# Performance work log

Measured on AMD Instinct MI355X. Metric: run time of the kernel, lower is better.

The kernel has to match this reference:

```python
import jax, jax.numpy as jnp
import numpy as np

N_NODES = 100000
N_EDGES = 1600000
D_IN, D_HID, N_CLS = 256, 128, 47


def setup_inputs() -> dict:
    key = jax.random.key(0)
    k = jax.random.split(key, 5)
    x = jax.random.normal(k[0], (N_NODES, D_IN), dtype=jnp.float32)
    edge_index = jax.random.randint(k[1], (2, N_EDGES), 0, N_NODES, dtype=jnp.int64)
    W1 = jax.random.normal(k[2], (D_IN, D_HID), dtype=jnp.float32) * 0.05
    b1 = jnp.zeros((D_HID,), dtype=jnp.float32)
    W2 = jax.random.normal(k[3], (D_HID, N_CLS), dtype=jnp.float32) * 0.05
    b2 = jnp.zeros((N_CLS,), dtype=jnp.float32)
    return {"x": x, "edge_index": edge_index, "W1": W1, "b1": b1, "W2": W2, "b2": b2}


def _gcn_conv(x, W, b, src, dst, norm, n):
    # PyG GCNConv: linear transform, normalized scatter-add aggregation, bias after
    h = x @ W                                   # [N, D_out]
    msg = h[src] * norm[:, None]                # gather over edges [E', D_out]
    agg = jax.ops.segment_sum(msg, dst, num_segments=n)
    return agg + b


def reference(x, edge_index, W1, b1, W2, b2):
    n = x.shape[0]
    loop = jnp.arange(n, dtype=edge_index.dtype)
    src = jnp.concatenate([edge_index[0], loop])  # add self-loops
    dst = jnp.concatenate([edge_index[1], loop])
    # symmetric normalization D^-1/2 (A+I) D^-1/2 (degree = in-degree incl. self-loop)
    deg = jax.ops.segment_sum(jnp.ones_like(dst, dtype=x.dtype), dst, num_segments=n)
    dinv = jnp.where(deg > 0, jax.lax.rsqrt(deg), 0.0)
    norm = dinv[src] * dinv[dst]                 # [E']
    h1 = jax.nn.relu(_gcn_conv(x, W1, b1, src, dst, norm, n))
    # dropout with training=False is identity
    out = _gcn_conv(h1, W2, b2, src, dst, norm, n)
    return out
```

## Files before the change

### kernel.cpp

```cpp
#include <hip/hip_runtime.h>
#include <hip/hip_bf16.h>

#define DIN 256
#define DHID 128
#define NCLS 47
#define BSHIFT 9
#define BNODES 512
#define NPART 256
#define BCAPS 9216
#define CHUNKE 6400

typedef __attribute__((ext_vector_type(8))) short short8;
typedef __attribute__((ext_vector_type(4))) float f32x4;

__device__ __forceinline__ short f2bf(float f) {
    __bf16 b = (__bf16)f;
    return __builtin_bit_cast(short, b);
}
__device__ __forceinline__ float bfu(unsigned int u) {
    return __uint_as_float(u << 16);
}
__device__ __forceinline__ float bfh(unsigned int u) {
    return __uint_as_float(u & 0xffff0000u);
}
__device__ __forceinline__ unsigned int pack2(float lo, float hi) {
    return (unsigned int)(unsigned short)f2bf(lo)
         | ((unsigned int)(unsigned short)f2bf(hi) << 16);
}
__device__ __forceinline__ void fma8(float* a, uint4 v, float d) {
    a[0] += d * bfu(v.x); a[1] += d * bfh(v.x);
    a[2] += d * bfu(v.y); a[3] += d * bfh(v.y);
    a[4] += d * bfu(v.z); a[5] += d * bfh(v.z);
    a[6] += d * bfu(v.w); a[7] += d * bfh(v.w);
}

__global__ __launch_bounds__(256) void k_prep_hist(const float* __restrict__ W1,
                                                   const float* __restrict__ W2,
                                                   short* __restrict__ W1s,
                                                   short* __restrict__ W2s,
                                                   const int* __restrict__ dst,
                                                   int* __restrict__ ghist,
                                                   int E, int NB, int chunk) {
    __shared__ int lh[256];
    int blk = blockIdx.x, t = threadIdx.x;
    if (blk < 16) {
        int tid = blk * 256 + t;
        int frag = tid >> 6, lane = tid & 63;
        int kt = frag >> 3, nt = frag & 7;
        int quad = lane >> 4, col = lane & 15;
        #pragma unroll
        for (int j = 0; j < 8; ++j) {
            int k = kt * 32 + quad * 8 + j;
            W1s[(size_t)tid * 8 + j] = f2bf(W1[k * DHID + nt * 16 + col]);
        }
    } else if (blk < 20) {
        int tid = (blk - 16) * 256 + t;
        int frag = tid >> 6, lane = tid & 63;
        int kt = frag >> 2, nt = frag & 3;
        int quad = lane >> 4, col = lane & 15;
        int c = nt * 16 + col;
        #pragma unroll
        for (int j = 0; j < 8; ++j) {
            int k = kt * 32 + quad * 8 + j;
            float v = (c < NCLS) ? W2[k * NCLS + c] : 0.0f;
            W2s[(size_t)tid * 8 + j] = f2bf(v);
        }
    } else {
        int p = blk - 20;
        for (int i = t; i < NB; i += 256) lh[i] = 0;
        __syncthreads();
        int lo = p * chunk, hi = min(E, lo + chunk);
        for (int i = lo + t; i < hi; i += 256)
            atomicAdd(&lh[dst[i] >> BSHIFT], 1);
        __syncthreads();
        for (int i = t; i < NB; i += 256) ghist[p * NB + i] = lh[i];
    }
}

__global__ __launch_bounds__(256) void k_scatter(const int* __restrict__ src,
                                                 const int* __restrict__ dst,
                                                 const int* __restrict__ ghist,
                                                 int* __restrict__ btot,
                                                 unsigned int* __restrict__ bbuf,
                                                 int E, int NB, int chunk) {
    __shared__ unsigned int stage[CHUNKE];
    __shared__ int sdest[CHUNKE];
    __shared__ int lcur[256];
    __shared__ int gdst[256];
    __shared__ int wsum[4];

    int blk = blockIdx.x, t = threadIdx.x;

    int tot = 0, pref = 0;
    if (t < NB) {
        #pragma unroll 8
        for (int p = 0; p < NPART; ++p) {
            int v = ghist[p * NB + t];
            tot += v;
            if (p < blk) pref += v;
        }
    }
    int mine = (t < NB) ? ghist[blk * NB + t] : 0;
    if (blk == 0 && t < NB) btot[t] = tot;

    int lane = t & 63, w = t >> 6;
    int incl = tot;
    #pragma unroll
    for (int off = 1; off < 64; off <<= 1) {
        int u = __shfl_up(incl, off, 64);
        if (lane >= off) incl += u;
    }
    if (lane == 63) wsum[w] = incl;
    __syncthreads();
    int wadd = 0;
    for (int i = 0; i < w; ++i) wadd += wsum[i];
    int bbase = wadd + incl - tot;
    __syncthreads();
    incl = mine;
    #pragma unroll
    for (int off = 1; off < 64; off <<= 1) {
        int u = __shfl_up(incl, off, 64);
        if (lane >= off) incl += u;
    }
    if (lane == 63) wsum[w] = incl;
    __syncthreads();
    wadd = 0;
    for (int i = 0; i < w; ++i) wadd += wsum[i];
    int ex = wadd + incl - mine;

    lcur[t] = ex;
    gdst[t] = bbase + pref - ex;
    __syncthreads();

    int lo = blk * chunk, hi = min(E, lo + chunk), cnt = hi - lo;
    for (int i = lo + t; i < hi; i += 256) {
        int d = dst[i];
        int b = d >> BSHIFT;
        int slot = atomicAdd(&lcur[b], 1);
        stage[slot] = (unsigned int)src[i] | ((unsigned int)(d & (BNODES - 1)) << 17);
        sdest[slot] = gdst[b] + slot;
    }
    __syncthreads();
    for (int i = t; i < cnt; i += 256)
        bbuf[sdest[i]] = stage[i];
}

__device__ __forceinline__ void scan_btot(const int* __restrict__ btot, int NB,
                                          int* lbase, int* wsum) {
    int t = threadIdx.x;
    int v = (t < NB) ? btot[t] : 0;
    int incl = v;
    int lane = t & 63, w = t >> 6;
    #pragma unroll
    for (int off = 1; off < 64; off <<= 1) {
        int u = __shfl_up(incl, off, 64);
        if (lane >= off) incl += u;
    }
    if (lane == 63) wsum[w] = incl;
    __syncthreads();
    int wadd = 0;
    for (int i = 0; i < w; ++i) wadd += wsum[i];
    lbase[t] = wadd + incl - v;
    __syncthreads();
}

__global__ __launch_bounds__(256) void k_bsort_gemm1(const int* __restrict__ btot,
                                                     unsigned int* __restrict__ bbuf,
                                                     int* __restrict__ degi,
                                                     int* __restrict__ beg,
                                                     float* __restrict__ dinv,
                                                     int n, int NB,
                                                     const float* __restrict__ x,
                                                     const short* __restrict__ W1s,
                                                     short* __restrict__ hb) {
    __shared__ __align__(16) char smem[65536];
    int blk = blockIdx.x, t = threadIdx.x;

    if (blk < NB) {
        unsigned int* stage = (unsigned int*)smem;
        int* hist  = (int*)(smem + 36864);
        int* cur   = (int*)(smem + 38912);
        int* lbase = (int*)(smem + 40960);
        int* wsum  = (int*)(smem + 41984);

        int b = blk;
        scan_btot(btot, NB, lbase, wsum);
        int cnt = min(btot[b], BCAPS);
        int gbase = lbase[b];
        int node0 = b << BSHIFT;

        if (t < 128) { ((int2*)hist)[t] = (int2){0, 0}; ((int2*)hist)[t + 128] = (int2){0, 0}; }
        __syncthreads();

        for (int i = t; i < cnt; i += 256) {
            unsigned int p = bbuf[gbase + i];
            stage[i] = p;
            atomicAdd(&hist[p >> 17], 1);
        }
        __syncthreads();

        int v0 = hist[2 * t], v1 = hist[2 * t + 1];
        int s = v0 + v1;
        int incl = s;
        int lane = t & 63, w = t >> 6;
        #pragma unroll
        for (int off = 1; off < 64; off <<= 1) {
            int u = __shfl_up(incl, off, 64);
            if (lane >= off) incl += u;
        }
        if (lane == 63) wsum[w] = incl;
        __syncthreads();
        int wadd = 0;
        for (int i = 0; i < w; ++i) wadd += wsum[i];
        int ex = wadd + incl - s;
        cur[2 * t] = ex;
        cur[2 * t + 1] = ex + v0;
        int nodeA = node0 + 2 * t, nodeB = node0 + 2 * t + 1;
        if (nodeA < n) {
            degi[nodeA] = v0;
            beg[nodeA]  = gbase + ex;
            dinv[nodeA] = rsqrtf((float)(v0 + 1));
        }
        if (nodeB < n) {
            degi[nodeB] = v1;
            beg[nodeB]  = gbase + ex + v0;
            dinv[nodeB] = rsqrtf((float)(v1 + 1));
        }
        __syncthreads();

        for (int i = t; i < cnt; i += 256) {
            unsigned int p = stage[i];
            int slot = atomicAdd(&cur[p >> 17], 1);
            bbuf[gbase + slot] = p & 0x1FFFFu;
        }
    } else {
        short* lw = (short*)smem;
        {
            const uint4* g = (const uint4*)W1s;
            uint4* l = (uint4*)lw;
            for (int i = t; i < 4096; i += 256) l[i] = g[i];
        }
        __syncthreads();

        int bid = blk - NB;
        int wave = t >> 6, lane = t & 63;
        int quad = lane >> 4, lrow = lane & 15;
        long long rowbase = (long long)bid * 128 + wave * 32;

        f32x4 acc[2][8];
        #pragma unroll
        for (int rt = 0; rt < 2; ++rt)
            #pragma unroll
            for (int nt = 0; nt < 8; ++nt) acc[rt][nt] = (f32x4){0.f, 0.f, 0.f, 0.f};

        const short8* lf = (const short8*)lw;

        #pragma unroll
        for (int kt = 0; kt < 8; ++kt) {
            int k0 = kt * 32 + quad * 8;
            short8 a[2];
            #pragma unroll
            for (int rt = 0; rt < 2; ++rt) {
                long long row = rowbase + rt * 16 + lrow;
                float4 v0 = {0.f,0.f,0.f,0.f}, v1 = {0.f,0.f,0.f,0.f};
                if (row < n) {
                    const float* xp = x + row * DIN + k0;
                    v0 = *(const float4*)xp;
                    v1 = *(const float4*)(xp + 4);
                }
                short8 av;
                av[0] = f2bf(v0.x); av[1] = f2bf(v0.y); av[2] = f2bf(v0.z); av[3] = f2bf(v0.w);
                av[4] = f2bf(v1.x); av[5] = f2bf(v1.y); av[6] = f2bf(v1.z); av[7] = f2bf(v1.w);
                a[rt] = av;
            }
            #pragma unroll
            for (int nt = 0; nt < 8; ++nt) {
                short8 b = lf[(kt * 8 + nt) * 64 + lane];
                acc[0][nt] = __builtin_amdgcn_mfma_f32_16x16x32_bf16(a[0], b, acc[0][nt], 0, 0, 0);
                acc[1][nt] = __builtin_amdgcn_mfma_f32_16x16x32_bf16(a[1], b, acc[1][nt], 0, 0, 0);
            }
        }
        #pragma unroll
        for (int rt = 0; rt < 2; ++rt)
            #pragma unroll
            for (int nt = 0; nt < 8; ++nt)
                #pragma unroll
                for (int r = 0; r < 4; ++r) {
                    long long row = rowbase + rt * 16 + quad * 4 + r;
                    if (row < n) hb[row * DHID + nt * 16 + lrow] = f2bf(acc[rt][nt][r]);
                }
    }
}

__global__ __launch_bounds__(256) void k_gather1(const int* __restrict__ beg,
                          const int* __restrict__ degi,
                          const int* __restrict__ ssrc, const float* __restrict__ dinv,
                          const uint4* __restrict__ hb4, const float* __restrict__ b1,
                          uint4* __restrict__ h1u4, int n) {
    int t = threadIdx.x & 63;
    int wv = threadIdx.x >> 6;
    int grp = t >> 4, sub = t & 15;
    int node = blockIdx.x * 16 + wv * 4 + grp;
    if (node >= n) return;
    int cnt = degi[node];
    int bg  = beg[node];

    float a[8] = {0.f,0.f,0.f,0.f,0.f,0.f,0.f,0.f};
    int k = 0;
    for (; k + 8 <= cnt; k += 8) {
        int s[8];
        #pragma unroll
        for (int q = 0; q < 8; ++q) s[q] = ssrc[bg + k + q];
        float dv[8]; uint4 v[8];
        #pragma unroll
        for (int q = 0; q < 8; ++q) { dv[q] = dinv[s[q]]; v[q] = hb4[(size_t)s[q] * 16 + sub]; }
        #pragma unroll
        for (int q = 0; q < 8; ++q) fma8(a, v[q], dv[q]);
    }
    #pragma unroll
    for (int q = 0; q < 8; ++q) {
        int idx = k + q;
        if (idx < cnt) {
            int s = ssrc[bg + idx];
            fma8(a, hb4[(size_t)s * 16 + sub], dinv[s]);
        }
    }
    uint4 sv = hb4[(size_t)node * 16 + sub];
    float di = dinv[node], dd = di * di;
    float4 bA = ((const float4*)b1)[sub * 2];
    float4 bB = ((const float4*)b1)[sub * 2 + 1];
    float v0 = fmaxf(di * a[0] + dd * bfu(sv.x) + bA.x, 0.f);
    float v1 = fmaxf(di * a[1] + dd * bfh(sv.x) + bA.y, 0.f);
    float v2 = fmaxf(di * a[2] + dd * bfu(sv.y) + bA.z, 0.f);
    float v3 = fmaxf(di * a[3] + dd * bfh(sv.y) + bA.w, 0.f);
    float v4 = fmaxf(di * a[4] + dd * bfu(sv.z) + bB.x, 0.f);
    float v5 = fmaxf(di * a[5] + dd * bfh(sv.z) + bB.y, 0.f);
    float v6 = fmaxf(di * a[6] + dd * bfu(sv.w) + bB.z, 0.f);
    float v7 = fmaxf(di * a[7] + dd * bfh(sv.w) + bB.w, 0.f);
    uint4 o;
    o.x = pack2(v0, v1);
    o.y = pack2(v2, v3);
    o.z = pack2(v4, v5);
    o.w = pack2(v6, v7);
    h1u4[(size_t)node * 16 + sub] = o;
}

__global__ __launch_bounds__(256) void k_gemm2_mfma(const short* __restrict__ h1b,
                                                    const short* __restrict__ W2s,
                                                    short* __restrict__ h2b, int n) {
    __shared__ short lw[8192];
    {
        const uint4* g = (const uint4*)W2s;
        uint4* l = (uint4*)lw;
        for (int i = threadIdx.x; i < 1024; i += 256) l[i] = g[i];
    }
    __syncthreads();

    int wave = threadIdx.x >> 6, lane = threadIdx.x & 63;
    int quad = lane >> 4, lrow = lane & 15;
    long long row0 = (long long)blockIdx.x * 64 + wave * 16;

    f32x4 acc[4];
    #pragma unroll
    for (int nt = 0; nt < 4; ++nt) acc[nt] = (f32x4){0.f, 0.f, 0.f, 0.f};

    const short8* lf = (const short8*)lw;

    #pragma unroll
    for (int kt = 0; kt < 4; ++kt) {
        long long row = row0 + lrow;
        short8 a = (short8){0,0,0,0,0,0,0,0};
        if (row < n) a = *(const short8*)(h1b + row * DHID + kt * 32 + quad * 8);
        #pragma unroll
        for (int nt = 0; nt < 4; ++nt)
            acc[nt] = __builtin_amdgcn_mfma_f32_16x16x32_bf16(a, lf[(kt * 4 + nt) * 64 + lane], acc[nt], 0, 0, 0);
    }
    #pragma unroll
    for (int nt = 0; nt < 4; ++nt)
        #pragma unroll
        for (int r = 0; r < 4; ++r) {
            long long row = row0 + quad * 4 + r;
            if (row < n) h2b[row * 64 + nt * 16 + lrow] = f2bf(acc[nt][r]);
        }
}

__global__ __launch_bounds__(256) void k_gather2(const int* __restrict__ beg,
                          const int* __restrict__ degi,
                          const int* __restrict__ ssrc, const float* __restrict__ dinv,
                          const uint4* __restrict__ h2b4, const float* __restrict__ b2,
                          float* __restrict__ out, int n) {
    int t = threadIdx.x & 63;
    int wv = threadIdx.x >> 6;
    int grp = t >> 3, sub = t & 7;
    int node = blockIdx.x * 32 + wv * 8 + grp;
    if (node >= n) return;
    int cnt = degi[node];
    int bg  = beg[node];

    float a[8] = {0.f,0.f,0.f,0.f,0.f,0.f,0.f,0.f};
    int k = 0;
    for (; k + 8 <= cnt; k += 8) {
        int s[8];
        #pragma unroll
        for (int q = 0; q < 8; ++q) s[q] = ssrc[bg + k + q];
        float dv[8]; uint4 v[8];
        #pragma unroll
        for (int q = 0; q < 8; ++q) { dv[q] = dinv[s[q]]; v[q] = h2b4[(size_t)s[q] * 8 + sub]; }
        #pragma unroll
        for (int q = 0; q < 8; ++q) fma8(a, v[q], dv[q]);
    }
    #pragma unroll
    for (int q = 0; q < 8; ++q) {
        int idx = k + q;
        if (idx < cnt) {
            int s = ssrc[bg + idx];
            fma8(a, h2b4[(size_t)s * 8 + sub], dinv[s]);
        }
    }
    uint4 sv = h2b4[(size_t)node * 8 + sub];
    float di = dinv[node], dd = di * di;
    float sf[8] = { bfu(sv.x), bfh(sv.x), bfu(sv.y), bfh(sv.y),
                    bfu(sv.z), bfh(sv.z), bfu(sv.w), bfh(sv.w) };
    #pragma unroll
    for (int j = 0; j < 8; ++j) {
        int c = sub * 8 + j;
        if (c < NCLS) out[(size_t)node * NCLS + c] = di * a[j] + dd * sf[j] + b2[c];
    }
}

extern "C" void kernel_launch(void* const* d_in, const int* in_sizes, int n_in,
                              void* d_out, int out_size, void* d_ws, size_t ws_size,
                              hipStream_t stream) {
    const float* x  = (const float*)d_in[0];
    const int*   ei = (const int*)d_in[1];
    const float* W1 = (const float*)d_in[2];
    const float* b1 = (const float*)d_in[3];
    const float* W2 = (const float*)d_in[4];
    const float* b2 = (const float*)d_in[5];

    const int n = in_sizes[0] / DIN;
    const int E = in_sizes[1] / 2;
    const int* src = ei;
    const int* dst = ei + E;
    float* out = (float*)d_out;

    const int NB = (n + BNODES - 1) >> BSHIFT;
    const int chunk = (E + NPART - 1) / NPART;

    char* w = (char*)d_ws;
    int*   ghist = (int*)w;                    w += (size_t)NPART * NB * 4;
    int*   btot  = (int*)w;                    w += ((size_t)NB * 4 + 15) & ~15ull;
    int*   degi  = (int*)w;                    w += (size_t)n * 4;
    int*   beg   = (int*)w;                    w += (size_t)n * 4;
    float* dinv  = (float*)w;                  w += (size_t)n * 4;
    short* W1s   = (short*)w;                  w += (size_t)32768 * 2;
    short* W2s   = (short*)w;                  w += (size_t)8192 * 2;
    unsigned int* bbuf = (unsigned int*)w;     w += (size_t)E * 4;
    short* hb    = (short*)w;                  w += (size_t)n * DHID * 2;
    short* h1b   = (short*)w;                  w += (size_t)n * DHID * 2;
    short* h2b   = (short*)w;                  w += (size_t)n * 64 * 2;

    k_prep_hist<<<20 + NPART, 256, 0, stream>>>(W1, W2, W1s, W2s, dst, ghist, E, NB, chunk);
    k_scatter<<<NPART, 256, 0, stream>>>(src, dst, ghist, btot, bbuf, E, NB, chunk);

    k_bsort_gemm1<<<NB + (n + 127) / 128, 256, 0, stream>>>(btot, bbuf, degi, beg, dinv,
                                                            n, NB, x, W1s, hb);

    k_gather1<<<(n + 15) / 16, 256, 0, stream>>>(beg, degi, (const int*)bbuf, dinv,
                                                 (const uint4*)hb, b1,
                                                 (uint4*)h1b, n);

    k_gemm2_mfma<<<(n + 63) / 64, 256, 0, stream>>>(h1b, W2s, h2b, n);
    k_gather2<<<(n + 31) / 32, 256, 0, stream>>>(beg, degi, (const int*)bbuf, dinv,
                                                 (const uint4*)h2b, b2, out, n);
}
```

Before: 408.8 us.

## Fuse gather1 with GEMM2, merge scatter with GEMM1, restructure gathers

GEMM1 now runs inside the scatter kernel instead of the bucket-sort kernel, and bucket sort becomes its own kernel. The layer-1 gather is fused with the layer-2 MFMA GEMM in a 1024-thread block, one node per wave, keeping h1 in shared memory so the h1b round trip through global memory goes away. The source-side dinv is folded into h2 at GEMM time, so gather2 becomes plain adds using one wave per node with shuffle reductions. The ghist layout is transposed so each bucket's per-partition counts are contiguous. In exchange, there are fewer nodes per wave and more shuffle reductions, and the 1024-thread blocks may lower occupancy.

```diff
diff --git a/kernel.cpp b/kernel.cpp
--- a/kernel.cpp
+++ b/kernel.cpp
@@ -26,6 +26,12 @@
 __device__ __forceinline__ unsigned int pack2(float lo, float hi) {
     return (unsigned int)(unsigned short)f2bf(lo)
          | ((unsigned int)(unsigned short)f2bf(hi) << 16);
+}
+__device__ __forceinline__ void add8(float* a, uint4 v) {
+    a[0] += bfu(v.x); a[1] += bfh(v.x);
+    a[2] += bfu(v.y); a[3] += bfh(v.y);
+    a[4] += bfu(v.z); a[5] += bfh(v.z);
+    a[6] += bfu(v.w); a[7] += bfh(v.w);
 }
 __device__ __forceinline__ void fma8(float* a, uint4 v, float d) {
     a[0] += d * bfu(v.x); a[1] += d * bfh(v.x);
@@ -73,136 +79,44 @@
         for (int i = lo + t; i < hi; i += 256)
             atomicAdd(&lh[dst[i] >> BSHIFT], 1);
         __syncthreads();
-        for (int i = t; i < NB; i += 256) ghist[p * NB + i] = lh[i];
-    }
-}
-
-__global__ __launch_bounds__(256) void k_scatter(const int* __restrict__ src,
-                                                 const int* __restrict__ dst,
-                                                 const int* __restrict__ ghist,
-                                                 int* __restrict__ btot,
-                                                 unsigned int* __restrict__ bbuf,
-                                                 int E, int NB, int chunk) {
-    __shared__ unsigned int stage[CHUNKE];
-    __shared__ int sdest[CHUNKE];
-    __shared__ int lcur[256];
-    __shared__ int gdst[256];
-    __shared__ int wsum[4];
-
-    int blk = blockIdx.x, t = threadIdx.x;
-
-    int tot = 0, pref = 0;
-    if (t < NB) {
-        #pragma unroll 8
-        for (int p = 0; p < NPART; ++p) {
-            int v = ghist[p * NB + t];
-            tot += v;
-            if (p < blk) pref += v;
-        }
-    }
-    int mine = (t < NB) ? ghist[blk * NB + t] : 0;
-    if (blk == 0 && t < NB) btot[t] = tot;
-
-    int lane = t & 63, w = t >> 6;
-    int incl = tot;
-    #pragma unroll
-    for (int off = 1; off < 64; off <<= 1) {
-        int u = __shfl_up(incl, off, 64);
-        if (lane >= off) incl += u;
-    }
-    if (lane == 63) wsum[w] = incl;
-    __syncthreads();
-    int wadd = 0;
-    for (int i = 0; i < w; ++i) wadd += wsum[i];
-    int bbase = wadd + incl - tot;
-    __syncthreads();
-    incl = mine;
-    #pragma unroll
-    for (int off = 1; off < 64; off <<= 1) {
-        int u = __shfl_up(incl, off, 64);
-        if (lane >= off) incl += u;
-    }
-    if (lane == 63) wsum[w] = incl;
-    __syncthreads();
-    wadd = 0;
-    for (int i = 0; i < w; ++i) wadd += wsum[i];
-    int ex = wadd + incl - mine;
-
-    lcur[t] = ex;
-    gdst[t] = bbase + pref - ex;
-    __syncthreads();
-
-    int lo = blk * chunk, hi = min(E, lo + chunk), cnt = hi - lo;
-    for (int i = lo + t; i < hi; i += 256) {
-        int d = dst[i];
-        int b = d >> BSHIFT;
-        int slot = atomicAdd(&lcur[b], 1);
-        stage[slot] = (unsigned int)src[i] | ((unsigned int)(d & (BNODES - 1)) << 17);
-        sdest[slot] = gdst[b] + slot;
-    }
-    __syncthreads();
-    for (int i = t; i < cnt; i += 256)
-        bbuf[sdest[i]] = stage[i];
-}
-
-__device__ __forceinline__ void scan_btot(const int* __restrict__ btot, int NB,
-                                          int* lbase, int* wsum) {
-    int t = threadIdx.x;
-    int v = (t < NB) ? btot[t] : 0;
-    int incl = v;
-    int lane = t & 63, w = t >> 6;
-    #pragma unroll
-    for (int off = 1; off < 64; off <<= 1) {
-        int u = __shfl_up(incl, off, 64);
-        if (lane >= off) incl += u;
-    }
-    if (lane == 63) wsum[w] = incl;
-    __syncthreads();
-    int wadd = 0;
-    for (int i = 0; i < w; ++i) wadd += wsum[i];
-    lbase[t] = wadd + incl - v;
-    __syncthreads();
-}
-
-__global__ __launch_bounds__(256) void k_bsort_gemm1(const int* __restrict__ btot,
-                                                     unsigned int* __restrict__ bbuf,
-                                                     int* __restrict__ degi,
-                                                     int* __restrict__ beg,
-                                                     float* __restrict__ dinv,
-                                                     int n, int NB,
-                                                     const float* __restrict__ x,
-                                                     const short* __restrict__ W1s,
-                                                     short* __restrict__ hb) {
+        for (int i = t; i < NB; i += 256) ghist[(size_t)i * NPART + p] = lh[i];
+    }
+}
+
+__global__ __launch_bounds__(256) void k_scatter_gemm1(const int* __restrict__ src,
+                                                       const int* __restrict__ dst,
+                                                       const int* __restrict__ ghist,
+                                                       int* __restrict__ btot,
+                                                       unsigned int* __restrict__ bbuf,
+                                                       int E, int NB, int chunk,
+                                                       const float* __restrict__ x,
+                                                       const short* __restrict__ W1s,
+                                                       short* __restrict__ hb, int n) {
     __shared__ __align__(16) char smem[65536];
     int blk = blockIdx.x, t = threadIdx.x;
 
-    if (blk < NB) {
+    if (blk < NPART) {
         unsigned int* stage = (unsigned int*)smem;
-        int* hist  = (int*)(smem + 36864);
-        int* cur   = (int*)(smem + 38912);
-        int* lbase = (int*)(smem + 40960);
-        int* wsum  = (int*)(smem + 41984);
-
-        int b = blk;
-        scan_btot(btot, NB, lbase, wsum);
-        int cnt = min(btot[b], BCAPS);
-        int gbase = lbase[b];
-        int node0 = b << BSHIFT;
-
-        if (t < 128) { ((int2*)hist)[t] = (int2){0, 0}; ((int2*)hist)[t + 128] = (int2){0, 0}; }
-        __syncthreads();
-
-        for (int i = t; i < cnt; i += 256) {
-            unsigned int p = bbuf[gbase + i];
-            stage[i] = p;
-            atomicAdd(&hist[p >> 17], 1);
-        }
-        __syncthreads();
-
-        int v0 = hist[2 * t], v1 = hist[2 * t + 1];
-        int s = v0 + v1;
-        int incl = s;
+        int* sdest = (int*)(smem + 25600);
+        int* lcur  = (int*)(smem + 51200);
+        int* gdst  = (int*)(smem + 52224);
+        int* wsum  = (int*)(smem + 53248);
+
+        int tot = 0, pref = 0, mine = 0;
+        if (t < NB) {
+            const int* gp = ghist + (size_t)t * NPART;
+            mine = gp[blk];
+            #pragma unroll 8
+            for (int p = 0; p < NPART; ++p) {
+                int v = gp[p];
+                tot += v;
+                pref += (p < blk) ? v : 0;
+            }
+        }
+        if (blk == 0 && t < NB) btot[t] = tot;
+
         int lane = t & 63, w = t >> 6;
+        int incl = tot;
         #pragma unroll
         for (int off = 1; off < 64; off <<= 1) {
             int u = __shfl_up(incl, off, 64);
@@ -212,27 +126,35 @@
         __syncthreads();
         int wadd = 0;
         for (int i = 0; i < w; ++i) wadd += wsum[i];
-        int ex = wadd + incl - s;
-        cur[2 * t] = ex;
-        cur[2 * t + 1] = ex + v0;
-        int nodeA = node0 + 2 * t, nodeB = node0 + 2 * t + 1;
-        if (nodeA < n) {
-            degi[nodeA] = v0;
-            beg[nodeA]  = gbase + ex;
-            dinv[nodeA] = rsqrtf((float)(v0 + 1));
-        }
-        if (nodeB < n) {
-            degi[nodeB] = v1;
-            beg[nodeB]  = gbase + ex + v0;
-            dinv[nodeB] = rsqrtf((float)(v1 + 1));
-        }
-        __syncthreads();
-
-        for (int i = t; i < cnt; i += 256) {
-            unsigned int p = stage[i];
-            int slot = atomicAdd(&cur[p >> 17], 1);
-            bbuf[gbase + slot] = p & 0x1FFFFu;
-        }
+        int bbase = wadd + incl - tot;
+        __syncthreads();
+        incl = mine;
+        #pragma unroll
+        for (int off = 1; off < 64; off <<= 1) {
+            int u = __shfl_up(incl, off, 64);
+            if (lane >= off) incl += u;
+        }
+        if (lane == 63) wsum[w] = incl;
+        __syncthreads();
+        wadd = 0;
+        for (int i = 0; i < w; ++i) wadd += wsum[i];
+        int ex = wadd + incl - mine;
+
+        lcur[t] = ex;
+        gdst[t] = bbase + pref - ex;
+        __syncthreads();
+
+        int lo = blk * chunk, hi = min(E, lo + chunk), cnt = hi - lo;
+        for (int i = lo + t; i < hi; i += 256) {
+            int d = dst[i];
+            int b = d >> BSHIFT;
+            int slot = atomicAdd(&lcur[b], 1);
+            stage[slot] = (unsigned int)src[i] | ((unsigned int)(d & (BNODES - 1)) << 17);
+            sdest[slot] = gdst[b] + slot;
+        }
+        __syncthreads();
+        for (int i = t; i < cnt; i += 256)
+            bbuf[sdest[i]] = stage[i];
     } else {
         short* lw = (short*)smem;
         {
@@ -242,7 +164,7 @@
         }
         __syncthreads();
 
-        int bid = blk - NB;
+        int bid = blk - NPART;
         int wave = t >> 6, lane = t & 63;
         int quad = lane >> 4, lrow = lane & 15;
         long long rowbase = (long long)bid * 128 + wave * 32;
@@ -292,96 +214,170 @@
     }
 }
 
-__global__ __launch_bounds__(256) void k_gather1(const int* __restrict__ beg,
+__device__ __forceinline__ void scan_btot(const int* __restrict__ btot, int NB,
+                                          int* lbase, int* wsum) {
+    int t = threadIdx.x;
+    int v = (t < NB) ? btot[t] : 0;
+    int incl = v;
+    int lane = t & 63, w = t >> 6;
+    #pragma unroll
+    for (int off = 1; off < 64; off <<= 1) {
+        int u = __shfl_up(incl, off, 64);
+        if (lane >= off) incl += u;
+    }
+    if (lane == 63) wsum[w] = incl;
+    __syncthreads();
+    int wadd = 0;
+    for (int i = 0; i < w; ++i) wadd += wsum[i];
+    lbase[t] = wadd + incl - v;
+    __syncthreads();
+}
+
+__global__ __launch_bounds__(256) void k_bsort(const int* __restrict__ btot,
+                                               unsigned int* __restrict__ bbuf,
+                                               int* __restrict__ degi,
+                                               int* __restrict__ beg,
+                                               float* __restrict__ dinv, int n, int NB) {
+    __shared__ unsigned int stage[BCAPS];
+    __shared__ int hist[BNODES];
+    __shared__ int cur[BNODES];
+    __shared__ int lbase[256];
+    __shared__ int wsum[4];
+
+    int b = blockIdx.x, t = threadIdx.x;
+    scan_btot(btot, NB, lbase, wsum);
+    int cnt = min(btot[b], BCAPS);
+    int gbase = lbase[b];
+    int node0 = b << BSHIFT;
+
+    if (t < 128) { ((int2*)hist)[t] = (int2){0, 0}; ((int2*)hist)[t + 128] = (int2){0, 0}; }
+    __syncthreads();
+
+    for (int i = t; i < cnt; i += 256) {
+        unsigned int p = bbuf[gbase + i];
+        stage[i] = p;
+        atomicAdd(&hist[p >> 17], 1);
+    }
+    __syncthreads();
+
+    int v0 = hist[2 * t], v1 = hist[2 * t + 1];
+    int s = v0 + v1;
+    int incl = s;
+    int lane = t & 63, w = t >> 6;
+    #pragma unroll
+    for (int off = 1; off < 64; off <<= 1) {
+        int u = __shfl_up(incl, off, 64);
+        if (lane >= off) incl += u;
+    }
+    if (lane == 63) wsum[w] = incl;
+    __syncthreads();
+    int wadd = 0;
+    for (int i = 0; i < w; ++i) wadd += wsum[i];
+    int ex = wadd + incl - s;
+    cur[2 * t] = ex;
+    cur[2 * t + 1] = ex + v0;
+    int nodeA = node0 + 2 * t, nodeB = node0 + 2 * t + 1;
+    if (nodeA < n) {
+        degi[nodeA] = v0;
+        beg[nodeA]  = gbase + ex;
+        dinv[nodeA] = rsqrtf((float)(v0 + 1));
+    }
+    if (nodeB < n) {
+        degi[nodeB] = v1;
+        beg[nodeB]  = gbase + ex + v0;
+        dinv[nodeB] = rsqrtf((float)(v1 + 1));
+    }
+    __syncthreads();
+
+    for (int i = t; i < cnt; i += 256) {
+        unsigned int p = stage[i];
+        int slot = atomicAdd(&cur[p >> 17], 1);
+        bbuf[gbase + slot] = p & 0x1FFFFu;
+    }
+}
+
+__global__ __launch_bounds__(1024) void k_g1g2(const int* __restrict__ beg,
                           const int* __restrict__ degi,
                           const int* __restrict__ ssrc, const float* __restrict__ dinv,
                           const uint4* __restrict__ hb4, const float* __restrict__ b1,
-                          uint4* __restrict__ h1u4, int n) {
-    int t = threadIdx.x & 63;
+                          const short* __restrict__ W2s,
+                          short* __restrict__ h2b, int n) {
+    __shared__ short lw[8192];
+    __shared__ short h1s[16 * 136];
+    ((uint4*)lw)[threadIdx.x & 1023] = ((const uint4*)W2s)[threadIdx.x & 1023];
+
     int wv = threadIdx.x >> 6;
+    int t  = threadIdx.x & 63;
     int grp = t >> 4, sub = t & 15;
-    int node = blockIdx.x * 16 + wv * 4 + grp;
-    if (node >= n) return;
-    int cnt = degi[node];
-    int bg  = beg[node];
+    int node = blockIdx.x * 16 + wv;
+    bool alive = node < n;
+    int cnt = alive ? degi[node] : 0;
+    int bg  = alive ? beg[node]  : 0;
 
     float a[8] = {0.f,0.f,0.f,0.f,0.f,0.f,0.f,0.f};
     int k = 0;
-    for (; k + 8 <= cnt; k += 8) {
-        int s[8];
-        #pragma unroll
-        for (int q = 0; q < 8; ++q) s[q] = ssrc[bg + k + q];
-        float dv[8]; uint4 v[8];
-        #pragma unroll
-        for (int q = 0; q < 8; ++q) { dv[q] = dinv[s[q]]; v[q] = hb4[(size_t)s[q] * 16 + sub]; }
-        #pragma unroll
-        for (int q = 0; q < 8; ++q) fma8(a, v[q], dv[q]);
-    }
-    #pragma unroll
-    for (int q = 0; q < 8; ++q) {
-        int idx = k + q;
+    for (; k + 16 <= cnt; k += 16) {
+        int s[4];
+        #pragma unroll
+        for (int q = 0; q < 4; ++q) s[q] = ssrc[bg + k + grp * 4 + q];
+        float dv[4]; uint4 v[4];
+        #pragma unroll
+        for (int q = 0; q < 4; ++q) { dv[q] = dinv[s[q]]; v[q] = hb4[(size_t)s[q] * 16 + sub]; }
+        #pragma unroll
+        for (int q = 0; q < 4; ++q) fma8(a, v[q], dv[q]);
+    }
+    for (; k < cnt; k += 4) {
+        int idx = k + grp;
         if (idx < cnt) {
             int s = ssrc[bg + idx];
             fma8(a, hb4[(size_t)s * 16 + sub], dinv[s]);
         }
     }
-    uint4 sv = hb4[(size_t)node * 16 + sub];
-    float di = dinv[node], dd = di * di;
-    float4 bA = ((const float4*)b1)[sub * 2];
-    float4 bB = ((const float4*)b1)[sub * 2 + 1];
-    float v0 = fmaxf(di * a[0] + dd * bfu(sv.x) + bA.x, 0.f);
-    float v1 = fmaxf(di * a[1] + dd * bfh(sv.x) + bA.y, 0.f);
-    float v2 = fmaxf(di * a[2] + dd * bfu(sv.y) + bA.z, 0.f);
-    float v3 = fmaxf(di * a[3] + dd * bfh(sv.y) + bA.w, 0.f);
-    float v4 = fmaxf(di * a[4] + dd * bfu(sv.z) + bB.x, 0.f);
-    float v5 = fmaxf(di * a[5] + dd * bfh(sv.z) + bB.y, 0.f);
-    float v6 = fmaxf(di * a[6] + dd * bfu(sv.w) + bB.z, 0.f);
-    float v7 = fmaxf(di * a[7] + dd * bfh(sv.w) + bB.w, 0.f);
-    uint4 o;
-    o.x = pack2(v0, v1);
-    o.y = pack2(v2, v3);
-    o.z = pack2(v4, v5);
-    o.w = pack2(v6, v7);
-    h1u4[(size_t)node * 16 + sub] = o;
-}
-
-__global__ __launch_bounds__(256) void k_gemm2_mfma(const short* __restrict__ h1b,
-                                                    const short* __restrict__ W2s,
-                                                    short* __restrict__ h2b, int n) {
-    __shared__ short lw[8192];
-    {
-        const uint4* g = (const uint4*)W2s;
-        uint4* l = (uint4*)lw;
-        for (int i = threadIdx.x; i < 1024; i += 256) l[i] = g[i];
-    }
-    __syncthreads();
-
-    int wave = threadIdx.x >> 6, lane = threadIdx.x & 63;
-    int quad = lane >> 4, lrow = lane & 15;
-    long long row0 = (long long)blockIdx.x * 64 + wave * 16;
-
-    f32x4 acc[4];
     #pragma unroll
-    for (int nt = 0; nt < 4; ++nt) acc[nt] = (f32x4){0.f, 0.f, 0.f, 0.f};
-
-    const short8* lf = (const short8*)lw;
-
-    #pragma unroll
-    for (int kt = 0; kt < 4; ++kt) {
-        long long row = row0 + lrow;
-        short8 a = (short8){0,0,0,0,0,0,0,0};
-        if (row < n) a = *(const short8*)(h1b + row * DHID + kt * 32 + quad * 8);
-        #pragma unroll
-        for (int nt = 0; nt < 4; ++nt)
-            acc[nt] = __builtin_amdgcn_mfma_f32_16x16x32_bf16(a, lf[(kt * 4 + nt) * 64 + lane], acc[nt], 0, 0, 0);
-    }
-    #pragma unroll
-    for (int nt = 0; nt < 4; ++nt)
+    for (int j = 0; j < 8; ++j) {
+        a[j] += __shfl_xor(a[j], 16);
+        a[j] += __shfl_xor(a[j], 32);
+    }
+
+    if (grp == 0) {
+        uint4 o = {0u, 0u, 0u, 0u};
+        if (alive) {
+            uint4 sv = hb4[(size_t)node * 16 + sub];
+            float di = dinv[node], dd = di * di;
+            float4 bA = ((const float4*)b1)[sub * 2];
+            float4 bB = ((const float4*)b1)[sub * 2 + 1];
+            float v0 = fmaxf(di * a[0] + dd * bfu(sv.x) + bA.x, 0.f);
+            float v1 = fmaxf(di * a[1] + dd * bfh(sv.x) + bA.y, 0.f);
+            float v2 = fmaxf(di * a[2] + dd * bfu(sv.y) + bA.z, 0.f);
+            float v3 = fmaxf(di * a[3] + dd * bfh(sv.y) + bA.w, 0.f);
+            float v4 = fmaxf(di * a[4] + dd * bfu(sv.z) + bB.x, 0.f);
+            float v5 = fmaxf(di * a[5] + dd * bfh(sv.z) + bB.y, 0.f);
+            float v6 = fmaxf(di * a[6] + dd * bfu(sv.w) + bB.z, 0.f);
+            float v7 = fmaxf(di * a[7] + dd * bfh(sv.w) + bB.w, 0.f);
+            o.x = pack2(v0, v1);
+            o.y = pack2(v2, v3);
+            o.z = pack2(v4, v5);
+            o.w = pack2(v6, v7);
+        }
+        *(uint4*)(h1s + wv * 136 + sub * 8) = o;
+    }
+    __syncthreads();
+
+    if (wv < 4) {
+        int quad = t >> 4, lrow = t & 15;
+        f32x4 acc = (f32x4){0.f, 0.f, 0.f, 0.f};
+        const short8* lf = (const short8*)lw;
+        #pragma unroll
+        for (int kt = 0; kt < 4; ++kt) {
+            short8 aa = *(const short8*)(h1s + lrow * 136 + kt * 32 + quad * 8);
+            acc = __builtin_amdgcn_mfma_f32_16x16x32_bf16(aa, lf[(kt * 4 + wv) * 64 + t], acc, 0, 0, 0);
+        }
         #pragma unroll
         for (int r = 0; r < 4; ++r) {
-            long long row = row0 + quad * 4 + r;
-            if (row < n) h2b[row * 64 + nt * 16 + lrow] = f2bf(acc[nt][r]);
-        }
+            int nodeo = blockIdx.x * 16 + quad * 4 + r;
+            if (nodeo < n) h2b[(size_t)nodeo * 64 + wv * 16 + lrow] = f2bf(acc[r] * dinv[nodeo]);
+        }
+    }
 }
 
 __global__ __launch_bounds__(256) void k_gather2(const int* __restrict__ beg,
@@ -389,42 +385,44 @@
                           const int* __restrict__ ssrc, const float* __restrict__ dinv,
                           const uint4* __restrict__ h2b4, const float* __restrict__ b2,
                           float* __restrict__ out, int n) {
+    int node = blockIdx.x * 4 + (threadIdx.x >> 6);
     int t = threadIdx.x & 63;
-    int wv = threadIdx.x >> 6;
-    int grp = t >> 3, sub = t & 7;
-    int node = blockIdx.x * 32 + wv * 8 + grp;
     if (node >= n) return;
     int cnt = degi[node];
     int bg  = beg[node];
+    int grp = t >> 3, sub = t & 7;
 
     float a[8] = {0.f,0.f,0.f,0.f,0.f,0.f,0.f,0.f};
     int k = 0;
-    for (; k + 8 <= cnt; k += 8) {
-        int s[8];
-        #pragma unroll
-        for (int q = 0; q < 8; ++q) s[q] = ssrc[bg + k + q];
-        float dv[8]; uint4 v[8];
-        #pragma unroll
-        for (int q = 0; q < 8; ++q) { dv[q] = dinv[s[q]]; v[q] = h2b4[(size_t)s[q] * 8 + sub]; }
-        #pragma unroll
-        for (int q = 0; q < 8; ++q) fma8(a, v[q], dv[q]);
-    }
-    #pragma unroll
-    for (int q = 0; q < 8; ++q) {
-        int idx = k + q;
+    for (; k + 16 <= cnt; k += 16) {
+        int s0 = ssrc[bg + k + grp], s1 = ssrc[bg + k + 8 + grp];
+        uint4 v0 = h2b4[(size_t)s0 * 8 + sub];
+        uint4 v1 = h2b4[(size_t)s1 * 8 + sub];
+        add8(a, v0); add8(a, v1);
+    }
+    for (; k < cnt; k += 8) {
+        int idx = k + grp;
         if (idx < cnt) {
             int s = ssrc[bg + idx];
-            fma8(a, h2b4[(size_t)s * 8 + sub], dinv[s]);
-        }
-    }
-    uint4 sv = h2b4[(size_t)node * 8 + sub];
-    float di = dinv[node], dd = di * di;
-    float sf[8] = { bfu(sv.x), bfh(sv.x), bfu(sv.y), bfh(sv.y),
-                    bfu(sv.z), bfh(sv.z), bfu(sv.w), bfh(sv.w) };
+            add8(a, h2b4[(size_t)s * 8 + sub]);
+        }
+    }
+    if (grp == 0) add8(a, h2b4[(size_t)node * 8 + sub]);
+
     #pragma unroll
     for (int j = 0; j < 8; ++j) {
-        int c = sub * 8 + j;
-        if (c < NCLS) out[(size_t)node * NCLS + c] = di * a[j] + dd * sf[j] + b2[c];
+        a[j] += __shfl_xor(a[j], 8);
+        a[j] += __shfl_xor(a[j], 16);
+        a[j] += __shfl_xor(a[j], 32);
+    }
+
+    if (grp == 0) {
+        float di = dinv[node];
+        #pragma unroll
+        for (int j = 0; j < 8; ++j) {
+            int c = sub * 8 + j;
+            if (c < NCLS) out[(size_t)node * NCLS + c] = di * a[j] + b2[c];
+        }
     }
 }
 
@@ -448,7 +446,7 @@
     const int chunk = (E + NPART - 1) / NPART;
 
     char* w = (char*)d_ws;
-    int*   ghist = (int*)w;                    w += (size_t)NPART * NB * 4;
+    int*   ghist = (int*)w;                    w += (size_t)NB * NPART * 4;
     int*   btot  = (int*)w;                    w += ((size_t)NB * 4 + 15) & ~15ull;
     int*   degi  = (int*)w;                    w += (size_t)n * 4;
     int*   beg   = (int*)w;                    w += (size_t)n * 4;
@@ -457,20 +455,14 @@
     short* W2s   = (short*)w;                  w += (size_t)8192 * 2;
     unsigned int* bbuf = (unsigned int*)w;     w += (size_t)E * 4;
     short* hb    = (short*)w;                  w += (size_t)n * DHID * 2;
-    short* h1b   = (short*)w;                  w += (size_t)n * DHID * 2;
     short* h2b   = (short*)w;                  w += (size_t)n * 64 * 2;
 
     k_prep_hist<<<20 + NPART, 256, 0, stream>>>(W1, W2, W1s, W2s, dst, ghist, E, NB, chunk);
-    k_scatter<<<NPART, 256, 0, stream>>>(src, dst, ghist, btot, bbuf, E, NB, chunk);
-
-    k_bsort_gemm1<<<NB + (n + 127) / 128, 256, 0, stream>>>(btot, bbuf, degi, beg, dinv,
-                                                            n, NB, x, W1s, hb);
-
-    k_gather1<<<(n + 15) / 16, 256, 0, stream>>>(beg, degi, (const int*)bbuf, dinv,
-                                                 (const uint4*)hb, b1,
-                                                 (uint4*)h1b, n);
-
-    k_gemm2_mfma<<<(n + 63) / 64, 256, 0, stream>>>(h1b, W2s, h2b, n);
-    k_gather2<<<(n + 31) / 32, 256, 0, stream>>>(beg, degi, (const int*)bbuf, dinv,
-                                                 (const uint4*)h2b, b2, out, n);
-}
+    k_scatter_gemm1<<<NPART + (n + 127) / 128, 256, 0, stream>>>(src, dst, ghist, btot, bbuf,
+                                                                 E, NB, chunk, x, W1s, hb, n);
+    k_bsort<<<NB, 256, 0, stream>>>(btot, bbuf, degi, beg, dinv, n, NB);
+    k_g1g2<<<(n + 15) / 16, 1024, 0, stream>>>(beg, degi, (const int*)bbuf, dinv,
+                                               (const uint4*)hb, b1, W2s, h2b, n);
+    k_gather2<<<(n + 3) / 4, 256, 0, stream>>>(beg, degi, (const int*)bbuf, dinv,
+                                               (const uint4*)h2b, b2, out, n);
+}
```

After: 409.6 us. No clear change (+0.2%).
